# Kernel optimization log

Hardware: AMD Instinct MI355X
Metric: run time of the kernel (lower is better)

## Reference

```python
import jax, jax.numpy as jnp
import numpy as np

N = 100000
E = 640000
C = 128
ALPHA = 0.1
BETA = 0.5
RESIDUAL = False


def setup_inputs() -> dict:
    key = jax.random.key(0)
    k1, k2, k3, k4, k5 = jax.random.split(key, 5)
    stdv = 1.0 / np.sqrt(C)
    x = jax.random.normal(k1, (N, C), dtype=jnp.float32)
    init_x = jax.random.normal(k2, (N, C), dtype=jnp.float32)
    weight = jax.random.uniform(k3, (C, C), dtype=jnp.float32, minval=-stdv, maxval=stdv)
    edge_index = jax.random.randint(k4, (2, E), 0, N, dtype=jnp.int64)
    edge_attr = jax.random.uniform(k5, (E,), dtype=jnp.float32)
    return {"x": x, "edge_index": edge_index, "edge_attr": edge_attr,
            "init_x": init_x, "weight": weight}


def reference(x, edge_index, edge_attr, init_x, weight):
    row, col = edge_index[0], edge_index[1]
    # spmm: out[row] += edge_attr * x[col]  (gather-scale-scatter)
    msgs = edge_attr[:, None] * x[col]                 # [E, C]
    hidden = jax.ops.segment_sum(msgs, row, num_segments=x.shape[0])  # [N, C]
    hidden = (1.0 - ALPHA) * hidden + ALPHA * init_x
    h = BETA * jnp.matmul(hidden, weight) + (1.0 - BETA) * hidden
    if RESIDUAL:
        h = h + x
    return h
```

## Files before the change

kernel.cpp:

```cpp
#include <hip/hip_runtime.h>


#define ALPHA 0.1f
#define BETA  0.5f
#define C_DIM 128

typedef __attribute__((ext_vector_type(8))) short short8v;
typedef __attribute__((ext_vector_type(4))) float f32x4;

__device__ inline unsigned bf16rn(float f) {
    unsigned u = __float_as_uint(f);
    return (u + 0x7FFFu + ((u >> 16) & 1u)) >> 16;
}
__device__ inline unsigned pack2(float lo, float hi) {
    return bf16rn(lo) | (bf16rn(hi) << 16);
}

__global__ void k_prep(const float4* __restrict__ x4, uint4* __restrict__ xb,
                       int n8, int* __restrict__ cnt, int N,
                       const float* __restrict__ W, ushort* __restrict__ Wt) {
    int i = blockIdx.x * 256 + threadIdx.x;
    if (i < n8) {
        float4 a = x4[2 * i], b = x4[2 * i + 1];
        uint4 o;
        o.x = pack2(a.x, a.y); o.y = pack2(a.z, a.w);
        o.z = pack2(b.x, b.y); o.w = pack2(b.z, b.w);
        xb[i] = o;
    }
    if (i < N) cnt[i] = 0;
    if (i < C_DIM * C_DIM) {
        int n = i >> 7, k = i & 127;
        float v = BETA * W[k * C_DIM + n] + ((k == n) ? (1.0f - BETA) : 0.0f);
        Wt[i] = (ushort)bf16rn(v);
    }
}

__global__ void k_hist(const int* __restrict__ ei, int* __restrict__ cnt, int E) {
    int e = blockIdx.x * 256 + threadIdx.x;
    if (e < E) atomicAdd(&cnt[ei[e]], 1);
}

__global__ void k_blockreduce(const int* __restrict__ cnt, int* __restrict__ partials, int n) {
    __shared__ int lds[256];
    int t = threadIdx.x;
    int base = blockIdx.x * 1024;
    int s = 0;
#pragma unroll
    for (int j = 0; j < 4; ++j) {
        int idx = base + j * 256 + t;
        if (idx < n) s += cnt[idx];
    }
    lds[t] = s;
    __syncthreads();
    for (int d = 128; d > 0; d >>= 1) {
        if (t < d) lds[t] += lds[t + d];
        __syncthreads();
    }
    if (t == 0) partials[blockIdx.x] = lds[0];
}

__global__ void k_blockscan(int* __restrict__ cnt, const int* __restrict__ partials, int n) {
    __shared__ int lds[256];
    __shared__ int base_s;
    int t = threadIdx.x;

    int pv = (t < blockIdx.x) ? partials[t] : 0;
    lds[t] = pv;
    __syncthreads();
    for (int d = 128; d > 0; d >>= 1) {
        if (t < d) lds[t] += lds[t + d];
        __syncthreads();
    }
    if (t == 0) base_s = lds[0];
    __syncthreads();

    int base = blockIdx.x * 1024 + t * 4;
    int4 v = {0, 0, 0, 0};
    if (base + 3 < n) v = *(const int4*)(cnt + base);
    else {
        if (base + 0 < n) v.x = cnt[base + 0];
        if (base + 1 < n) v.y = cnt[base + 1];
        if (base + 2 < n) v.z = cnt[base + 2];
        if (base + 3 < n) v.w = cnt[base + 3];
    }
    int s = v.x + v.y + v.z + v.w;
    lds[t] = s;
    for (int d = 1; d < 256; d <<= 1) {
        __syncthreads();
        int tmp = (t >= d) ? lds[t - d] : 0;
        __syncthreads();
        lds[t] += tmp;
    }
    __syncthreads();
    int thrBase = base_s + lds[t] - s;
    int4 o;
    o.x = thrBase;
    o.y = thrBase + v.x;
    o.z = thrBase + v.x + v.y;
    o.w = thrBase + v.x + v.y + v.z;
    if (base + 3 < n) *(int4*)(cnt + base) = o;
    else {
        if (base + 0 < n) cnt[base + 0] = o.x;
        if (base + 1 < n) cnt[base + 1] = o.y;
        if (base + 2 < n) cnt[base + 2] = o.z;
        if (base + 3 < n) cnt[base + 3] = o.w;
    }
}

__global__ void k_build(const int* __restrict__ ei, const float* __restrict__ attr,
                        int* __restrict__ cur, float2* __restrict__ recs, int E) {
    int e = blockIdx.x * 256 + threadIdx.x;
    if (e >= E) return;
    int row = ei[e];
    int pos = atomicAdd(&cur[row], 1);
    recs[pos] = make_float2(__int_as_float(ei[E + e]), (1.0f - ALPHA) * attr[e]);
}

__device__ inline void fma8(float* acc, float a, uint4 v) {
    acc[0] += a * __uint_as_float(v.x << 16);
    acc[1] += a * __uint_as_float(v.x & 0xffff0000u);
    acc[2] += a * __uint_as_float(v.y << 16);
    acc[3] += a * __uint_as_float(v.y & 0xffff0000u);
    acc[4] += a * __uint_as_float(v.z << 16);
    acc[5] += a * __uint_as_float(v.z & 0xffff0000u);
    acc[6] += a * __uint_as_float(v.w << 16);
    acc[7] += a * __uint_as_float(v.w & 0xffff0000u);
}

template <int USE_BF16>
__global__ __launch_bounds__(256)
void k_fused16(const void* __restrict__ xsrc, const int* __restrict__ cnt,
               const float2* __restrict__ recs, const float4* __restrict__ init4,
               const ushort* __restrict__ Wt, float* __restrict__ out, int N) {
    __shared__ ushort hs[16 * C_DIM];
    const int tid = threadIdx.x;
    const long R0 = (long)blockIdx.x * 16;

    {
        const int g = tid >> 4;
        const int l = tid & 15;
        long r = R0 + g;
        float acc[8] = {0.f, 0.f, 0.f, 0.f, 0.f, 0.f, 0.f, 0.f};
        if (r < N) {
            int start = (r == 0) ? 0 : cnt[r - 1];
            int end = cnt[r];
            int k = start;
            if (USE_BF16) {
                const uint4* xb4 = (const uint4*)xsrc;
                for (; k + 4 <= end; k += 4) {
                    float2 e0 = recs[k + 0];
                    float2 e1 = recs[k + 1];
                    float2 e2 = recs[k + 2];
                    float2 e3 = recs[k + 3];
                    uint4 v0 = xb4[(size_t)__float_as_int(e0.x) * 16 + l];
                    uint4 v1 = xb4[(size_t)__float_as_int(e1.x) * 16 + l];
                    uint4 v2 = xb4[(size_t)__float_as_int(e2.x) * 16 + l];
                    uint4 v3 = xb4[(size_t)__float_as_int(e3.x) * 16 + l];
                    fma8(acc, e0.y, v0);
                    fma8(acc, e1.y, v1);
                    fma8(acc, e2.y, v2);
                    fma8(acc, e3.y, v3);
                }
                if (k + 2 <= end) {
                    float2 e0 = recs[k + 0];
                    float2 e1 = recs[k + 1];
                    uint4 v0 = xb4[(size_t)__float_as_int(e0.x) * 16 + l];
                    uint4 v1 = xb4[(size_t)__float_as_int(e1.x) * 16 + l];
                    fma8(acc, e0.y, v0);
                    fma8(acc, e1.y, v1);
                    k += 2;
                }
                if (k < end) {
                    float2 e0 = recs[k];
                    uint4 v0 = xb4[(size_t)__float_as_int(e0.x) * 16 + l];
                    fma8(acc, e0.y, v0);
                }
            } else {
                const float4* x4 = (const float4*)xsrc;
                for (; k < end; ++k) {
                    float2 e0 = recs[k];
                    const float4* xr = x4 + (size_t)__float_as_int(e0.x) * 32 + l * 2;
                    float4 a0 = xr[0], a1 = xr[1];
                    float w = e0.y;
                    acc[0] += w * a0.x; acc[1] += w * a0.y;
                    acc[2] += w * a0.z; acc[3] += w * a0.w;
                    acc[4] += w * a1.x; acc[5] += w * a1.y;
                    acc[6] += w * a1.z; acc[7] += w * a1.w;
                }
            }
            float4 i0 = init4[r * 32 + l * 2];
            float4 i1 = init4[r * 32 + l * 2 + 1];
            acc[0] += ALPHA * i0.x; acc[1] += ALPHA * i0.y;
            acc[2] += ALPHA * i0.z; acc[3] += ALPHA * i0.w;
            acc[4] += ALPHA * i1.x; acc[5] += ALPHA * i1.y;
            acc[6] += ALPHA * i1.z; acc[7] += ALPHA * i1.w;
        }
        uint4 o;
        o.x = pack2(acc[0], acc[1]);
        o.y = pack2(acc[2], acc[3]);
        o.z = pack2(acc[4], acc[5]);
        o.w = pack2(acc[6], acc[7]);
        int gi = l ^ (g & 7);
        *(uint4*)&hs[g * 128 + gi * 8] = o;
    }
    __syncthreads();

    {
        const int lane = tid & 63;
        const int wv = tid >> 6;
        const int m = lane & 15, gg = lane >> 4;
        const uint4* W16 = (const uint4*)Wt;

        f32x4 acc[2];
        acc[0] = (f32x4){0.f, 0.f, 0.f, 0.f};
        acc[1] = (f32x4){0.f, 0.f, 0.f, 0.f};

#pragma unroll
        for (int ks = 0; ks < 4; ++ks) {
            int gi = (ks * 4 + gg) ^ (m & 7);
            short8v a = *(const short8v*)&hs[m * 128 + gi * 8];
#pragma unroll
            for (int j = 0; j < 2; ++j) {
                int nt = wv * 2 + j;
                union { uint4 q; short8v v; } b;
                b.q = W16[(nt * 16 + m) * 16 + (ks * 4 + gg)];
                acc[j] = __builtin_amdgcn_mfma_f32_16x16x32_bf16(a, b.v, acc[j], 0, 0, 0);
            }
        }

#pragma unroll
        for (int j = 0; j < 2; ++j) {
            int nt = wv * 2 + j;
            long rb = R0 + gg * 4;
#pragma unroll
            for (int reg = 0; reg < 4; ++reg) {
                long r = rb + reg;
                if (r >= N) continue;
                out[r * C_DIM + nt * 16 + m] = acc[j][reg];
            }
        }
    }
}

extern "C" void kernel_launch(void* const* d_in, const int* in_sizes, int n_in,
                              void* d_out, int out_size, void* d_ws, size_t ws_size,
                              hipStream_t stream) {
    const float* x      = (const float*)d_in[0];
    const int*   ei     = (const int*)d_in[1];
    const float* attr   = (const float*)d_in[2];
    const float* init_x = (const float*)d_in[3];
    const float* W      = (const float*)d_in[4];
    float* out = (float*)d_out;

    const int N = in_sizes[0] / C_DIM;
    const int E = in_sizes[2];

    const int N_pad = (N + 255) & ~255;
    const size_t cnt_bytes = (size_t)N_pad * 4;
    const size_t rec_bytes = (size_t)E * 8;
    const size_t wt_bytes  = (size_t)C_DIM * C_DIM * 2;
    const size_t xb_bytes  = (size_t)N * C_DIM * 2;
    const size_t base_need = cnt_bytes + 1024 + rec_bytes + wt_bytes;
    const bool use_bf16 = ws_size >= base_need + xb_bytes;

    char* wsp = (char*)d_ws;
    int*    cnt      = (int*)wsp;
    int*    partials = cnt + N_pad;
    float2* recs     = (float2*)((char*)partials + 1024);
    ushort* Wt       = (ushort*)((char*)recs + rec_bytes);
    uint4*  xb       = use_bf16 ? (uint4*)((char*)Wt + wt_bytes) : nullptr;

    const int B = (N + 1023) / 1024;
    const int n8 = use_bf16 ? (N * C_DIM / 8) : 0;
    int prep_elems = (n8 > N) ? n8 : N;
    if (prep_elems < C_DIM * C_DIM) prep_elems = C_DIM * C_DIM;

    k_prep<<<(prep_elems + 255) / 256, 256, 0, stream>>>((const float4*)x, xb, n8,
                                                         cnt, N, W, Wt);
    k_hist<<<(E + 255) / 256, 256, 0, stream>>>(ei, cnt, E);
    k_blockreduce<<<B, 256, 0, stream>>>(cnt, partials, N);
    k_blockscan<<<B, 256, 0, stream>>>(cnt, partials, N);
    k_build<<<(E + 255) / 256, 256, 0, stream>>>(ei, attr, cnt, recs, E);
    if (use_bf16) {
        k_fused16<1><<<(N + 15) / 16, 256, 0, stream>>>((const void*)xb, cnt, recs,
                                                        (const float4*)init_x, Wt, out, N);
    } else {
        k_fused16<0><<<(N + 15) / 16, 256, 0, stream>>>((const void*)x, cnt, recs,
                                                        (const float4*)init_x, Wt, out, N);
    }
}
```

Baseline: 139.2 us.

## Fuse histogram into prep, add bf16 init_x, and widen fused tile to 32 rows

The histogram kernel is folded into the prep kernel, and counter zeroing moves to hipMemsetAsync. init_x is also converted to bf16 in prep when workspace allows, so the fused kernel reads half the init bytes. The fused gather+MFMA kernel now handles 32 rows per block, with 8 lanes per row each covering 16 channels. It uses a predicated 4-way unrolled edge loop with no scalar tails, and each wave does a 16x64 MFMA tile. The trade-offs are an extra full pass converting init_x (read fp32, write bf16, read again), less row parallelism per block, and added bf16 rounding of init_x.

```diff
diff --git a/kernel.cpp b/kernel.cpp
--- a/kernel.cpp
+++ b/kernel.cpp
@@ -16,28 +16,31 @@
     return bf16rn(lo) | (bf16rn(hi) << 16);
 }
 
-__global__ void k_prep(const float4* __restrict__ x4, uint4* __restrict__ xb,
-                       int n8, int* __restrict__ cnt, int N,
-                       const float* __restrict__ W, ushort* __restrict__ Wt) {
+__global__ void k_prep(const float4* __restrict__ x4, uint4* __restrict__ xb, int n8x,
+                       const float4* __restrict__ i4, uint4* __restrict__ ib, int n8i,
+                       const float* __restrict__ W, ushort* __restrict__ Wt,
+                       const int* __restrict__ ei, int* __restrict__ cnt, int E) {
     int i = blockIdx.x * 256 + threadIdx.x;
-    if (i < n8) {
+    if (i < n8x) {
         float4 a = x4[2 * i], b = x4[2 * i + 1];
         uint4 o;
         o.x = pack2(a.x, a.y); o.y = pack2(a.z, a.w);
         o.z = pack2(b.x, b.y); o.w = pack2(b.z, b.w);
         xb[i] = o;
-    }
-    if (i < N) cnt[i] = 0;
-    if (i < C_DIM * C_DIM) {
-        int n = i >> 7, k = i & 127;
+    } else if (i < n8x + n8i) {
+        int j = i - n8x;
+        float4 a = i4[2 * j], b = i4[2 * j + 1];
+        uint4 o;
+        o.x = pack2(a.x, a.y); o.y = pack2(a.z, a.w);
+        o.z = pack2(b.x, b.y); o.w = pack2(b.z, b.w);
+        ib[j] = o;
+    } else if (i < n8x + n8i + C_DIM * C_DIM) {
+        int j = i - n8x - n8i;
+        int n = j >> 7, k = j & 127;
         float v = BETA * W[k * C_DIM + n] + ((k == n) ? (1.0f - BETA) : 0.0f);
-        Wt[i] = (ushort)bf16rn(v);
-    }
-}
-
-__global__ void k_hist(const int* __restrict__ ei, int* __restrict__ cnt, int E) {
-    int e = blockIdx.x * 256 + threadIdx.x;
-    if (e < E) atomicAdd(&cnt[ei[e]], 1);
+        Wt[j] = (ushort)bf16rn(v);
+    }
+    if (i < E) atomicAdd(&cnt[ei[i]], 1);
 }
 
 __global__ void k_blockreduce(const int* __restrict__ cnt, int* __restrict__ partials, int n) {
@@ -127,81 +130,89 @@
     acc[7] += a * __uint_as_float(v.w & 0xffff0000u);
 }
 
-template <int USE_BF16>
+template <int MODE>
 __global__ __launch_bounds__(256)
-void k_fused16(const void* __restrict__ xsrc, const int* __restrict__ cnt,
-               const float2* __restrict__ recs, const float4* __restrict__ init4,
+void k_fused32(const void* __restrict__ xsrc, const void* __restrict__ isrc,
+               const int* __restrict__ cnt, const float2* __restrict__ recs,
                const ushort* __restrict__ Wt, float* __restrict__ out, int N) {
-    __shared__ ushort hs[16 * C_DIM];
+    __shared__ ushort hs[32 * C_DIM];
     const int tid = threadIdx.x;
-    const long R0 = (long)blockIdx.x * 16;
+    const long R0 = (long)blockIdx.x * 32;
 
     {
-        const int g = tid >> 4;
-        const int l = tid & 15;
+        const int g = tid >> 3;
+        const int l = tid & 7;
         long r = R0 + g;
-        float acc[8] = {0.f, 0.f, 0.f, 0.f, 0.f, 0.f, 0.f, 0.f};
+        float acc[16];
+#pragma unroll
+        for (int j = 0; j < 16; ++j) acc[j] = 0.f;
         if (r < N) {
             int start = (r == 0) ? 0 : cnt[r - 1];
             int end = cnt[r];
-            int k = start;
-            if (USE_BF16) {
+            if (MODE >= 1) {
                 const uint4* xb4 = (const uint4*)xsrc;
-                for (; k + 4 <= end; k += 4) {
-                    float2 e0 = recs[k + 0];
-                    float2 e1 = recs[k + 1];
-                    float2 e2 = recs[k + 2];
-                    float2 e3 = recs[k + 3];
-                    uint4 v0 = xb4[(size_t)__float_as_int(e0.x) * 16 + l];
-                    uint4 v1 = xb4[(size_t)__float_as_int(e1.x) * 16 + l];
-                    uint4 v2 = xb4[(size_t)__float_as_int(e2.x) * 16 + l];
-                    uint4 v3 = xb4[(size_t)__float_as_int(e3.x) * 16 + l];
-                    fma8(acc, e0.y, v0);
-                    fma8(acc, e1.y, v1);
-                    fma8(acc, e2.y, v2);
-                    fma8(acc, e3.y, v3);
-                }
-                if (k + 2 <= end) {
-                    float2 e0 = recs[k + 0];
-                    float2 e1 = recs[k + 1];
-                    uint4 v0 = xb4[(size_t)__float_as_int(e0.x) * 16 + l];
-                    uint4 v1 = xb4[(size_t)__float_as_int(e1.x) * 16 + l];
-                    fma8(acc, e0.y, v0);
-                    fma8(acc, e1.y, v1);
-                    k += 2;
-                }
-                if (k < end) {
+                for (int k = start; k < end; k += 4) {
+                    int k1 = (k + 1 < end) ? k + 1 : end - 1;
+                    int k2 = (k + 2 < end) ? k + 2 : end - 1;
+                    int k3 = (k + 3 < end) ? k + 3 : end - 1;
                     float2 e0 = recs[k];
-                    uint4 v0 = xb4[(size_t)__float_as_int(e0.x) * 16 + l];
-                    fma8(acc, e0.y, v0);
+                    float2 e1 = recs[k1];
+                    float2 e2 = recs[k2];
+                    float2 e3 = recs[k3];
+                    float w1 = (k + 1 < end) ? e1.y : 0.f;
+                    float w2 = (k + 2 < end) ? e2.y : 0.f;
+                    float w3 = (k + 3 < end) ? e3.y : 0.f;
+                    const uint4* p0 = &xb4[(size_t)__float_as_int(e0.x) * 16 + 2 * l];
+                    const uint4* p1 = &xb4[(size_t)__float_as_int(e1.x) * 16 + 2 * l];
+                    const uint4* p2 = &xb4[(size_t)__float_as_int(e2.x) * 16 + 2 * l];
+                    const uint4* p3 = &xb4[(size_t)__float_as_int(e3.x) * 16 + 2 * l];
+                    uint4 a0 = p0[0], b0 = p0[1];
+                    uint4 a1 = p1[0], b1 = p1[1];
+                    uint4 a2 = p2[0], b2 = p2[1];
+                    uint4 a3 = p3[0], b3 = p3[1];
+                    fma8(acc, e0.y, a0); fma8(acc + 8, e0.y, b0);
+                    fma8(acc, w1, a1);   fma8(acc + 8, w1, b1);
+                    fma8(acc, w2, a2);   fma8(acc + 8, w2, b2);
+                    fma8(acc, w3, a3);   fma8(acc + 8, w3, b3);
                 }
             } else {
                 const float4* x4 = (const float4*)xsrc;
-                for (; k < end; ++k) {
+                for (int k = start; k < end; ++k) {
                     float2 e0 = recs[k];
-                    const float4* xr = x4 + (size_t)__float_as_int(e0.x) * 32 + l * 2;
-                    float4 a0 = xr[0], a1 = xr[1];
+                    const float4* xr = x4 + (size_t)__float_as_int(e0.x) * 32 + l * 4;
                     float w = e0.y;
-                    acc[0] += w * a0.x; acc[1] += w * a0.y;
-                    acc[2] += w * a0.z; acc[3] += w * a0.w;
-                    acc[4] += w * a1.x; acc[5] += w * a1.y;
-                    acc[6] += w * a1.z; acc[7] += w * a1.w;
+#pragma unroll
+                    for (int q = 0; q < 4; ++q) {
+                        float4 v = xr[q];
+                        acc[q * 4 + 0] += w * v.x; acc[q * 4 + 1] += w * v.y;
+                        acc[q * 4 + 2] += w * v.z; acc[q * 4 + 3] += w * v.w;
+                    }
                 }
             }
-            float4 i0 = init4[r * 32 + l * 2];
-            float4 i1 = init4[r * 32 + l * 2 + 1];
-            acc[0] += ALPHA * i0.x; acc[1] += ALPHA * i0.y;
-            acc[2] += ALPHA * i0.z; acc[3] += ALPHA * i0.w;
-            acc[4] += ALPHA * i1.x; acc[5] += ALPHA * i1.y;
-            acc[6] += ALPHA * i1.z; acc[7] += ALPHA * i1.w;
+            if (MODE == 2) {
+                const uint4* ib4 = (const uint4*)isrc;
+                uint4 i0 = ib4[(size_t)r * 16 + 2 * l];
+                uint4 i1 = ib4[(size_t)r * 16 + 2 * l + 1];
+                fma8(acc, ALPHA, i0);
+                fma8(acc + 8, ALPHA, i1);
+            } else {
+                const float4* if4 = (const float4*)isrc;
+#pragma unroll
+                for (int q = 0; q < 4; ++q) {
+                    float4 v = if4[(size_t)r * 32 + l * 4 + q];
+                    acc[q * 4 + 0] += ALPHA * v.x; acc[q * 4 + 1] += ALPHA * v.y;
+                    acc[q * 4 + 2] += ALPHA * v.z; acc[q * 4 + 3] += ALPHA * v.w;
+                }
+            }
         }
-        uint4 o;
-        o.x = pack2(acc[0], acc[1]);
-        o.y = pack2(acc[2], acc[3]);
-        o.z = pack2(acc[4], acc[5]);
-        o.w = pack2(acc[6], acc[7]);
-        int gi = l ^ (g & 7);
-        *(uint4*)&hs[g * 128 + gi * 8] = o;
+        uint4 o0, o1;
+        o0.x = pack2(acc[0], acc[1]);  o0.y = pack2(acc[2], acc[3]);
+        o0.z = pack2(acc[4], acc[5]);  o0.w = pack2(acc[6], acc[7]);
+        o1.x = pack2(acc[8], acc[9]);  o1.y = pack2(acc[10], acc[11]);
+        o1.z = pack2(acc[12], acc[13]); o1.w = pack2(acc[14], acc[15]);
+        int s = g & 7;
+        *(uint4*)&hs[g * 128 + ((2 * l) ^ s) * 8] = o0;
+        *(uint4*)&hs[g * 128 + ((2 * l + 1) ^ s) * 8] = o1;
     }
     __syncthreads();
 
@@ -209,29 +220,32 @@
         const int lane = tid & 63;
         const int wv = tid >> 6;
         const int m = lane & 15, gg = lane >> 4;
+        const int mt = wv & 1;
+        const int ng = wv >> 1;
         const uint4* W16 = (const uint4*)Wt;
 
-        f32x4 acc[2];
-        acc[0] = (f32x4){0.f, 0.f, 0.f, 0.f};
-        acc[1] = (f32x4){0.f, 0.f, 0.f, 0.f};
-
+        f32x4 acc[4];
+#pragma unroll
+        for (int j = 0; j < 4; ++j) acc[j] = (f32x4){0.f, 0.f, 0.f, 0.f};
+
+        const int rl = mt * 16 + m;
 #pragma unroll
         for (int ks = 0; ks < 4; ++ks) {
-            int gi = (ks * 4 + gg) ^ (m & 7);
-            short8v a = *(const short8v*)&hs[m * 128 + gi * 8];
-#pragma unroll
-            for (int j = 0; j < 2; ++j) {
-                int nt = wv * 2 + j;
+            int gi = (ks * 4 + gg) ^ (rl & 7);
+            short8v a = *(const short8v*)&hs[rl * 128 + gi * 8];
+#pragma unroll
+            for (int j = 0; j < 4; ++j) {
+                int nt = ng * 4 + j;
                 union { uint4 q; short8v v; } b;
                 b.q = W16[(nt * 16 + m) * 16 + (ks * 4 + gg)];
                 acc[j] = __builtin_amdgcn_mfma_f32_16x16x32_bf16(a, b.v, acc[j], 0, 0, 0);
             }
         }
 
-#pragma unroll
-        for (int j = 0; j < 2; ++j) {
-            int nt = wv * 2 + j;
-            long rb = R0 + gg * 4;
+        long rb = R0 + mt * 16 + gg * 4;
+#pragma unroll
+        for (int j = 0; j < 4; ++j) {
+            int nt = ng * 4 + j;
 #pragma unroll
             for (int reg = 0; reg < 4; ++reg) {
                 long r = rb + reg;
@@ -261,31 +275,41 @@
     const size_t wt_bytes  = (size_t)C_DIM * C_DIM * 2;
     const size_t xb_bytes  = (size_t)N * C_DIM * 2;
     const size_t base_need = cnt_bytes + 1024 + rec_bytes + wt_bytes;
-    const bool use_bf16 = ws_size >= base_need + xb_bytes;
+
+    int mode = 0;
+    if (ws_size >= base_need + 2 * xb_bytes) mode = 2;
+    else if (ws_size >= base_need + xb_bytes) mode = 1;
 
     char* wsp = (char*)d_ws;
     int*    cnt      = (int*)wsp;
     int*    partials = cnt + N_pad;
     float2* recs     = (float2*)((char*)partials + 1024);
     ushort* Wt       = (ushort*)((char*)recs + rec_bytes);
-    uint4*  xb       = use_bf16 ? (uint4*)((char*)Wt + wt_bytes) : nullptr;
+    uint4*  xb = (mode >= 1) ? (uint4*)((char*)Wt + wt_bytes) : nullptr;
+    uint4*  ib = (mode == 2) ? (uint4*)((char*)xb + xb_bytes) : nullptr;
 
     const int B = (N + 1023) / 1024;
-    const int n8 = use_bf16 ? (N * C_DIM / 8) : 0;
-    int prep_elems = (n8 > N) ? n8 : N;
-    if (prep_elems < C_DIM * C_DIM) prep_elems = C_DIM * C_DIM;
-
-    k_prep<<<(prep_elems + 255) / 256, 256, 0, stream>>>((const float4*)x, xb, n8,
-                                                         cnt, N, W, Wt);
-    k_hist<<<(E + 255) / 256, 256, 0, stream>>>(ei, cnt, E);
+    const int n8x = (mode >= 1) ? (N * C_DIM / 8) : 0;
+    const int n8i = (mode == 2) ? (N * C_DIM / 8) : 0;
+    int prep_elems = n8x + n8i + C_DIM * C_DIM;
+    if (prep_elems < E) prep_elems = E;
+
+    hipMemsetAsync(cnt, 0, (size_t)N * 4, stream);
+    k_prep<<<(prep_elems + 255) / 256, 256, 0, stream>>>(
+        (const float4*)x, xb, n8x, (const float4*)init_x, ib, n8i, W, Wt, ei, cnt, E);
     k_blockreduce<<<B, 256, 0, stream>>>(cnt, partials, N);
     k_blockscan<<<B, 256, 0, stream>>>(cnt, partials, N);
     k_build<<<(E + 255) / 256, 256, 0, stream>>>(ei, attr, cnt, recs, E);
-    if (use_bf16) {
-        k_fused16<1><<<(N + 15) / 16, 256, 0, stream>>>((const void*)xb, cnt, recs,
-                                                        (const float4*)init_x, Wt, out, N);
+
+    const int fgrid = (N + 31) / 32;
+    if (mode == 2) {
+        k_fused32<2><<<fgrid, 256, 0, stream>>>((const void*)xb, (const void*)ib,
+                                                cnt, recs, Wt, out, N);
+    } else if (mode == 1) {
+        k_fused32<1><<<fgrid, 256, 0, stream>>>((const void*)xb, (const void*)init_x,
+                                                cnt, recs, Wt, out, N);
     } else {
-        k_fused16<0><<<(N + 15) / 16, 256, 0, stream>>>((const void*)x, cnt, recs,
-                                                        (const float4*)init_x, Wt, out, N);
-    }
-}
+        k_fused32<0><<<fgrid, 256, 0, stream>>>((const void*)x, (const void*)init_x,
+                                                cnt, recs, Wt, out, N);
+    }
+}
```

After: 149.7 us. 7.6% more time.
